# Performance work log

Measured on AMD Instinct MI355X. Metric: run time of the kernel, lower is better.

## Reference

```python
import jax, jax.numpy as jnp
import numpy as np

HEADS, K = 8, 32
EPS = 1e-5


def bn(x, gamma, beta):
    # batch-stat BN over all axes except the last (channel) axis
    axes = tuple(range(x.ndim - 1))
    m = jnp.mean(x, axes, keepdims=True)
    v = jnp.var(x, axes, keepdims=True)
    return (x - m) / jnp.sqrt(v + EPS) * gamma + beta


def leaky(z):
    return jax.nn.leaky_relu(z, 0.2)


def conv1(t, W, g, b):  # 1x1 Conv1d + BN + LeakyReLU, channels-last
    return leaky(bn(jnp.einsum('bnc,dc->bnd', t, W), g, b))


def conv2(t, W, g, b):  # 1x1 Conv2d + BN + LeakyReLU on (B,N,k,C)
    return leaky(bn(jnp.einsum('bnkc,dc->bnkd', t, W), g, b))


def _forward(x, pos, Wq, gq, bq, Wk, gk, bk, Wv, gv, bv,
             Wpb, gpb, bpb, We1, ge1, be1, We2, ge2, be2,
             Wm1, gm1, bm1, Wm2, gm2, bm2):
    B, N, C = x.shape
    cph = C // HEADS
    q = conv1(x, Wq, gq, bq)
    key = conv1(x, Wk, gk, bk)
    val = conv1(x, Wv, gv, bv)
    # kNN in key-feature space (DGCNN-style get_graph_feature, edge_function='global')
    sq = jnp.sum(key * key, -1)                          # (B,N)
    dist = sq[:, :, None] + sq[:, None, :] - 2.0 * jnp.einsum('bnc,bmc->bnm', key, key)
    _, idx = jax.lax.top_k(-dist, K)                     # (B,N,K)
    bidx = jnp.arange(B)[:, None, None]
    key_nb = key[bidx, idx]                              # (B,N,K,C)
    val_nb = val[bidx, idx]
    pos_nb = pos[bidx, idx]
    mask = jnp.sign(idx + 1).astype(x.dtype)             # (B,N,K), all ones for valid knn
    masked_pos = (pos_nb - pos[:, :, None, :]) * mask[..., None]
    posb = conv2(masked_pos, Wpb, gpb, bpb)              # (B,N,K,C)
    vector = key_nb - q[:, :, None, :] + posb            # vector attention logits input
    value = val_nb + posb
    vector = conv2(conv2(vector, We1, ge1, be1), We2, ge2, be2)  # (B,N,K,cph)
    vector = jax.nn.softmax(vector, axis=2) * mask[..., None]    # softmax over k neighbors
    value = value.reshape(B, N, K, cph, HEADS)
    attn = jnp.einsum('bnkgh,bnkg->bngh', value, vector).reshape(B, N, C)
    x = x + attn
    h = jax.nn.silu(bn(jnp.einsum('bnc,dc->bnd', x, Wm1), gm1, bm1))
    m = jax.nn.silu(bn(jnp.einsum('bnc,dc->bnd', h, Wm2), gm2, bm2))
    return x + m


def setup_inputs():
    key = jax.random.key(0)
    ks = jax.random.split(key, 16)
    B, N, C, H = 2, 2048, 256, 512
    cph = C // HEADS
    s = 0.02
    inp = {
        'x': jax.random.normal(ks[0], (B, N, C), jnp.float32),
        'pos': jax.random.normal(ks[1], (B, N, C), jnp.float32),
        'Wq': jax.random.normal(ks[2], (C, C), jnp.float32) * s,
        'gq': jnp.ones((C,), jnp.float32), 'bq': jnp.zeros((C,), jnp.float32),
        'Wk': jax.random.normal(ks[3], (C, C), jnp.float32) * s,
        'gk': jnp.ones((C,), jnp.float32), 'bk': jnp.zeros((C,), jnp.float32),
        'Wv': jax.random.normal(ks[4], (C, C), jnp.float32) * s,
        'gv': jnp.ones((C,), jnp.float32), 'bv': jnp.zeros((C,), jnp.float32),
        'Wpb': jax.random.normal(ks[5], (C, C), jnp.float32) * s,
        'gpb': jnp.ones((C,), jnp.float32), 'bpb': jnp.zeros((C,), jnp.float32),
        'We1': jax.random.normal(ks[6], (cph, C), jnp.float32) * s,
        'ge1': jnp.ones((cph,), jnp.float32), 'be1': jnp.zeros((cph,), jnp.float32),
        'We2': jax.random.normal(ks[7], (cph, cph), jnp.float32) * s,
        'ge2': jnp.ones((cph,), jnp.float32), 'be2': jnp.zeros((cph,), jnp.float32),
        'Wm1': jax.random.normal(ks[8], (H, C), jnp.float32) * s,
        'gm1': jnp.ones((H,), jnp.float32), 'bm1': jnp.zeros((H,), jnp.float32),
        'Wm2': jax.random.normal(ks[9], (C, H), jnp.float32) * s,
        'gm2': jnp.ones((C,), jnp.float32), 'bm2': jnp.zeros((C,), jnp.float32),
    }
    return inp


def reference(x, pos, Wq, gq, bq, Wk, gk, bk, Wv, gv, bv,
              Wpb, gpb, bpb, We1, ge1, be1, We2, ge2, be2,
              Wm1, gm1, bm1, Wm2, gm2, bm2):
    return _forward(x, pos, Wq, gq, bq, Wk, gk, bk, Wv, gv, bv,
                    Wpb, gpb, bpb, We1, ge1, be1, We2, ge2, be2,
                    Wm1, gm1, bm1, Wm2, gm2, bm2)
```

## Files before the change

kernel.cpp:

```cpp
#include <hip/hip_runtime.h>

#define EPS 1e-5f

typedef __attribute__((ext_vector_type(8))) short s8v;
typedef __attribute__((ext_vector_type(4))) float f4v;

__device__ __forceinline__ float leakyf(float z){ return z >= 0.f ? z : 0.2f*z; }
__device__ __forceinline__ float siluf(float y){ return y / (1.f + __expf(-y)); }
__device__ __forceinline__ unsigned f2bfu(float f){
  unsigned u = __float_as_uint(f);
  return (u + 0x7FFFu + ((u>>16)&1u)) >> 16;
}
__device__ __forceinline__ unsigned short bfr(float f){ return (unsigned short)f2bfu(f); }
__device__ __forceinline__ float bf2f16(unsigned short s){ return __uint_as_float(((unsigned)s)<<16); }

__global__ __launch_bounds__(256) void k_zero(float* __restrict__ p, int n){
  int i = blockIdx.x*256 + threadIdx.x;
  if (i < n) p[i] = 0.f;
}

template<bool TRANSA, bool STATS, bool FULL4>
__global__ __launch_bounds__(256) void k_gemm(
    const float* __restrict__ A, int lda, long aStr,
    const float* __restrict__ A3, int lda3,
    const float* __restrict__ fAbuck, float invnA, int CA,
    const float* __restrict__ gA, const float* __restrict__ bA,
    const float* __restrict__ B0, const float* __restrict__ B1,
    const float* __restrict__ B2, const float* __restrict__ B3, int ldb, long bStr,
    float* __restrict__ C, int ldc, long cStr,
    float* __restrict__ C3, int ldc3,
    int K, float* __restrict__ buck, int statC, int statChanStr)
{
  __shared__ unsigned short Ah[2048], Al[2048], Bh[2048], Bl[2048];
  __shared__ float Ssum[STATS?64:4], Ssq[STATS?64:4];
  __shared__ float mrA[TRANSA?1024:4];
  const int z = blockIdx.z;
  const bool zAlt = (A3 != nullptr) && (z == 3);
  const float* Az = zAlt ? A3 : A + (long)z*aStr;
  const int ldaz = zAlt ? lda3 : lda;
  const float* Bb = (z==0?B0 : z==1?B1 : (z==2?B2:B3)) + (long)z*bStr;
  float* Cb = zAlt ? C3 : (C + (long)z*cStr);
  const int ldcz = zAlt ? ldc3 : ldc;
  const bool doStats = STATS && !zAlt;
  const int tid = threadIdx.x;
  const int bm = blockIdx.x*64, bn = blockIdx.y*64;
  const int wv = tid>>6, lane = tid&63;
  const int lm = lane&15, quad = lane>>4;
  if (doStats && tid<64){ Ssum[tid]=0.f; Ssq[tid]=0.f; }
  if (TRANSA){
    for (int c = tid; c < CA; c += 256){
      float s=0.f, q=0.f;
      for (int b=0;b<64;b++){ s += fAbuck[(long)b*2*CA + c]; q += fAbuck[(long)b*2*CA + CA + c]; }
      float m = s*invnA;
      float v = fmaxf(q*invnA - m*m, 0.f);
      mrA[c] = m; mrA[CA + c] = rsqrtf(v + EPS);
    }
    __syncthreads();
  }

  const int r0 = tid>>3, kg = tid&7;
  const int qk = kg>>1, j0 = (kg&1)*4;
  const int s0 = ((((r0>>4)  )*4 + qk)*16 + ((r0&15)^qk))*8 + j0;
  const int s1 = ((((r0>>4)+2)*4 + qk)*16 + ((r0&15)^qk))*8 + j0;
  const float* aP0 = Az + (long)(bm+r0)*ldaz + kg*4;
  const float* aP1 = aP0 + (long)32*ldaz;
  const float* bP0 = Bb + (long)(bn+r0)*ldb + kg*4;
  const float* bP1 = bP0 + (long)32*ldb;

  f4v acc[4];
  #pragma unroll
  for (int j=0;j<4;j++) acc[j] = (f4v){0.f,0.f,0.f,0.f};

  float4 a0 = *(const float4*)(aP0);
  float4 a1 = *(const float4*)(aP1);
  float4 b0 = *(const float4*)(bP0);
  float4 b1 = *(const float4*)(bP1);

  for (int k0=0; k0<K; k0+=32){
    float4 av0 = a0, av1 = a1;
    if (TRANSA){
      float4 m4 = *(const float4*)&mrA[k0 + kg*4];
      float4 r4 = *(const float4*)&mrA[CA + k0 + kg*4];
      float4 g4 = *(const float4*)(gA + k0 + kg*4);
      float4 b4 = *(const float4*)(bA + k0 + kg*4);
      av0.x = siluf((av0.x - m4.x)*r4.x*g4.x + b4.x);
      av0.y = siluf((av0.y - m4.y)*r4.y*g4.y + b4.y);
      av0.z = siluf((av0.z - m4.z)*r4.z*g4.z + b4.z);
      av0.w = siluf((av0.w - m4.w)*r4.w*g4.w + b4.w);
      av1.x = siluf((av1.x - m4.x)*r4.x*g4.x + b4.x);
      av1.y = siluf((av1.y - m4.y)*r4.y*g4.y + b4.y);
      av1.z = siluf((av1.z - m4.z)*r4.z*g4.z + b4.z);
      av1.w = siluf((av1.w - m4.w)*r4.w*g4.w + b4.w);
    }
    ushort4 h4, l4;
    h4.x=bfr(av0.x); l4.x=bfr(av0.x-bf2f16(h4.x));
    h4.y=bfr(av0.y); l4.y=bfr(av0.y-bf2f16(h4.y));
    h4.z=bfr(av0.z); l4.z=bfr(av0.z-bf2f16(h4.z));
    h4.w=bfr(av0.w); l4.w=bfr(av0.w-bf2f16(h4.w));
    *(ushort4*)&Ah[s0]=h4; *(ushort4*)&Al[s0]=l4;
    h4.x=bfr(av1.x); l4.x=bfr(av1.x-bf2f16(h4.x));
    h4.y=bfr(av1.y); l4.y=bfr(av1.y-bf2f16(h4.y));
    h4.z=bfr(av1.z); l4.z=bfr(av1.z-bf2f16(h4.z));
    h4.w=bfr(av1.w); l4.w=bfr(av1.w-bf2f16(h4.w));
    *(ushort4*)&Ah[s1]=h4; *(ushort4*)&Al[s1]=l4;
    h4.x=bfr(b0.x); l4.x=bfr(b0.x-bf2f16(h4.x));
    h4.y=bfr(b0.y); l4.y=bfr(b0.y-bf2f16(h4.y));
    h4.z=bfr(b0.z); l4.z=bfr(b0.z-bf2f16(h4.z));
    h4.w=bfr(b0.w); l4.w=bfr(b0.w-bf2f16(h4.w));
    *(ushort4*)&Bh[s0]=h4; *(ushort4*)&Bl[s0]=l4;
    h4.x=bfr(b1.x); l4.x=bfr(b1.x-bf2f16(h4.x));
    h4.y=bfr(b1.y); l4.y=bfr(b1.y-bf2f16(h4.y));
    h4.z=bfr(b1.z); l4.z=bfr(b1.z-bf2f16(h4.z));
    h4.w=bfr(b1.w); l4.w=bfr(b1.w-bf2f16(h4.w));
    *(ushort4*)&Bh[s1]=h4; *(ushort4*)&Bl[s1]=l4;
    __syncthreads();
    if (k0+32 < K){
      a0 = *(const float4*)(aP0 + k0+32);
      a1 = *(const float4*)(aP1 + k0+32);
      b0 = *(const float4*)(bP0 + k0+32);
      b1 = *(const float4*)(bP1 + k0+32);
    }
    const int soA = ((wv*4 + quad)*16 + (lm^quad))*8;
    s8v ah = *(const s8v*)&Ah[soA];
    s8v al = *(const s8v*)&Al[soA];
    #pragma unroll
    for (int j=0;j<4;j++){
      const int soB = ((j*4 + quad)*16 + (lm^quad))*8;
      s8v bh = *(const s8v*)&Bh[soB];
      s8v bl = *(const s8v*)&Bl[soB];
      acc[j] = __builtin_amdgcn_mfma_f32_16x16x32_bf16(ah, bh, acc[j], 0,0,0);
      acc[j] = __builtin_amdgcn_mfma_f32_16x16x32_bf16(ah, bl, acc[j], 0,0,0);
      acc[j] = __builtin_amdgcn_mfma_f32_16x16x32_bf16(al, bh, acc[j], 0,0,0);
      if (FULL4)
        acc[j] = __builtin_amdgcn_mfma_f32_16x16x32_bf16(al, bl, acc[j], 0,0,0);
    }
    __syncthreads();
  }
  #pragma unroll
  for (int rr=0;rr<4;rr++){
    float* cr = Cb + (long)(bm + wv*16 + quad*4 + rr)*ldcz + bn + lm;
    #pragma unroll
    for (int j=0;j<4;j++) cr[j*16] = acc[j][rr];
  }
  if (doStats){
    #pragma unroll
    for (int j=0;j<4;j++){
      float s=0.f, q=0.f;
      #pragma unroll
      for (int rr=0;rr<4;rr++){ float v = acc[j][rr]; s += v; q += v*v; }
      s += __shfl_xor(s,16,64); s += __shfl_xor(s,32,64);
      q += __shfl_xor(q,16,64); q += __shfl_xor(q,32,64);
      if (quad==0){ atomicAdd(&Ssum[j*16+lm], s); atomicAdd(&Ssq[j*16+lm], q); }
    }
    __syncthreads();
    if (tid < 64){
      int chan = statChanStr*z + bn + tid;
      float* bb = buck + (long)(blockIdx.x & 63)*2*statC;
      atomicAdd(&bb[chan], Ssum[tid]);
      atomicAdd(&bb[statC + chan], Ssq[tid]);
    }
  }
}

__global__ void k_finalize(const float* __restrict__ buck, int C, float invn, float* __restrict__ mr){
  int c = blockIdx.x*256 + threadIdx.x;
  if (c < C){
    float s=0,q=0;
    for (int b=0;b<64;b++){ s += buck[(long)b*2*C + c]; q += buck[(long)b*2*C + C + c]; }
    float m = s*invn;
    float v = fmaxf(q*invn - m*m, 0.f);
    mr[c] = m; mr[C+c] = rsqrtf(v + EPS);
  }
}

__global__ __launch_bounds__(256) void k_apply_qkv(const float* __restrict__ raw, const float* __restrict__ bQKV,
    const float* __restrict__ gq, const float* __restrict__ bq,
    const float* __restrict__ gk, const float* __restrict__ bk,
    const float* __restrict__ gv, const float* __restrict__ bv,
    float* __restrict__ key, float* __restrict__ qv, float* __restrict__ sq){
  __shared__ float mrs[1536];
  __shared__ float red[4];
  const int tid = threadIdx.x;
  const int wv = tid>>6, lane = tid&63;
  for (int c = tid; c < 768; c += 256){
    float s=0.f, q=0.f;
    for (int b=0;b<64;b++){ s += bQKV[(long)b*1536 + c]; q += bQKV[(long)b*1536 + 768 + c]; }
    float m = s*(1.f/4096.f);
    float v = fmaxf(q*(1.f/4096.f) - m*m, 0.f);
    mrs[c] = m; mrs[768+c] = rsqrtf(v + EPS);
  }
  __syncthreads();
  const float gqv = gq[tid], bqv = bq[tid], gkv = gk[tid], bkv = bk[tid], gvv = gv[tid], bvv = bv[tid];
  for (int rr=0; rr<8; rr++){
    const long r = (long)blockIdx.x*8 + rr;
    const float* row = raw + r*768;
    float zq = row[tid], zk = row[256+tid], zv = row[512+tid];
    float yq = leakyf((zq - mrs[tid])*mrs[768+tid]*gqv + bqv);
    float yk = leakyf((zk - mrs[256+tid])*mrs[1024+tid]*gkv + bkv);
    float yv = leakyf((zv - mrs[512+tid])*mrs[1280+tid]*gvv + bvv);
    qv[r*512 + tid] = yq;
    key[r*256 + tid] = yk;
    qv[r*512 + 256 + tid] = yv;
    float kq = yk*yk;
    kq += __shfl_xor(kq,1,64); kq += __shfl_xor(kq,2,64);
    kq += __shfl_xor(kq,4,64); kq += __shfl_xor(kq,8,64);
    kq += __shfl_xor(kq,16,64); kq += __shfl_xor(kq,32,64);
    if (lane==0) red[wv] = kq;
    __syncthreads();
    if (tid==0) sq[r] = red[0]+red[1]+red[2]+red[3];
    __syncthreads();
  }
}

__global__ __launch_bounds__(256) void k_topk(const float* __restrict__ G2, const float* __restrict__ sq,
    int* __restrict__ idxb, const float* __restrict__ P, float* __restrict__ bPB){
  __shared__ float dist[4][2048];
  const int wv = threadIdx.x >> 6, lane = threadIdx.x & 63;
  const int row = blockIdx.x*4 + wv;
  const int b = row >> 11, n = row & 2047;
  const float* Grow = G2 + (long)b*4194304 + (long)n*2048;
  const float* sqb = sq + b*2048;
  const float sqn = sqb[n];
  float lmin = 3.4e38f; int lidx = 0;
  for (int j=0;j<32;j++){
    int m = lane + j*64;
    float d = sqn + sqb[m] - 2.f*Grow[m];
    dist[wv][m] = d;
    if (d < lmin){ lmin = d; lidx = m; }
  }
  int* orow = idxb + row*32;
  int myidx[32];
  for (int t=0;t<32;t++){
    float v = lmin; int i = lidx;
    for (int off=32; off; off>>=1){
      float v2 = __shfl_xor(v, off, 64);
      int i2 = __shfl_xor(i, off, 64);
      if (v2 < v || (v2 == v && i2 < i)){ v = v2; i = i2; }
    }
    myidx[t] = i;
    if (lane == 0) orow[t] = i;
    if ((i & 63) == lane){
      dist[wv][i] = 3.4e38f;
      lmin = 3.4e38f; lidx = 0;
      for (int j=0;j<32;j++){
        int m = lane + j*64;
        float d = dist[wv][m];
        if (d < lmin){ lmin = d; lidx = m; }
      }
    }
  }
  const long base = (long)b << 11;
  const int c4 = lane*4;
  float4 pn = *(const float4*)(P + (long)row*256 + c4);
  float s0=0,s1=0,s2=0,s3=0,q0=0,q1=0,q2=0,q3=0;
  for (int t=0;t<32;t++){
    float4 pg = *(const float4*)(P + (base + myidx[t])*256 + c4);
    float z0 = pg.x - pn.x, z1 = pg.y - pn.y, z2 = pg.z - pn.z, z3 = pg.w - pn.w;
    s0+=z0; q0+=z0*z0; s1+=z1; q1+=z1*z1;
    s2+=z2; q2+=z2*z2; s3+=z3; q3+=z3*z3;
  }
  float* bb = bPB + (long)(blockIdx.x & 63)*512;
  atomicAdd(&bb[c4+0], s0); atomicAdd(&bb[c4+1], s1);
  atomicAdd(&bb[c4+2], s2); atomicAdd(&bb[c4+3], s3);
  atomicAdd(&bb[256+c4+0], q0); atomicAdd(&bb[256+c4+1], q1);
  atomicAdd(&bb[256+c4+2], q2); atomicAdd(&bb[256+c4+3], q3);
}

__global__ __launch_bounds__(256) void k_e1m(
    const float* __restrict__ key, const float* __restrict__ qv, const float* __restrict__ P,
    const int* __restrict__ idx, const float* __restrict__ mrPB,
    const float* __restrict__ gpb, const float* __restrict__ bpb,
    const float* __restrict__ We1, float* __restrict__ E1, float* __restrict__ buckE1)
{
  __shared__ unsigned short Ab[16384];
  __shared__ unsigned short Wb[8192];
  __shared__ float Ssum[32], Ssq[32];
  const int tid = threadIdx.x;
  const int wv = tid>>6, lane = tid&63;
  const int quad = lane>>4, lm = lane&15;
  const int bn0 = blockIdx.x*2;
  if (tid < 32){ Ssum[tid]=0.f; Ssq[tid]=0.f; }
  for (int e = tid; e < 8192; e += 256){
    int d = e >> 8, c = e & 255;
    int off = (((d>>4)*8 + (c>>5))*4 + ((c>>3)&3))*128 + (d&15)*8 + (c&7);
    Wb[off] = bfr(We1[e]);
  }
  {
    const int bn = bn0 + (wv>>1);
    const long base = (long)(bn >> 11) << 11;
    const int c4 = lane*4;
    float4 q4  = *(const float4*)(qv + (long)bn*512 + c4);
    float4 pn4 = *(const float4*)(P + (long)bn*256 + c4);
    float4 mp4 = *(const float4*)(mrPB + c4);
    float4 rp4 = *(const float4*)(mrPB + 256 + c4);
    float4 g4  = *(const float4*)(gpb + c4);
    float4 b4  = *(const float4*)(bpb + c4);
    const int ksc = c4>>5, quadc = (c4>>3)&3, jc = c4&7;
    for (int j = 0; j < 16; ++j){
      const int rloc = wv*16 + j;
      const int kk = rloc & 31;
      const int g = idx[bn*32 + kk];
      float4 kb = *(const float4*)(key + (base+g)*256 + c4);
      float4 pb = *(const float4*)(P + (base+g)*256 + c4);
      float o0 = kb.x - q4.x + leakyf((pb.x - pn4.x - mp4.x)*rp4.x*g4.x + b4.x);
      float o1 = kb.y - q4.y + leakyf((pb.y - pn4.y - mp4.y)*rp4.y*g4.y + b4.y);
      float o2 = kb.z - q4.z + leakyf((pb.z - pn4.z - mp4.z)*rp4.z*g4.z + b4.z);
      float o3 = kb.w - q4.w + leakyf((pb.w - pn4.w - mp4.w)*rp4.w*g4.w + b4.w);
      const int atile = rloc >> 4;
      const int slot = ((rloc & 15) ^ (ksc<<1) ^ quadc) & 15;
      const int off = ((atile*8 + ksc)*4 + quadc)*128 + slot*8 + jc;
      ushort4 u; u.x = bfr(o0); u.y = bfr(o1); u.z = bfr(o2); u.w = bfr(o3);
      *(ushort4*)&Ab[off] = u;
    }
  }
  __syncthreads();
  f4v acc0 = (f4v){0,0,0,0}, acc1 = (f4v){0,0,0,0};
  #pragma unroll
  for (int ks=0; ks<8; ks++){
    const int aslot = (lm ^ (ks<<1) ^ quad) & 15;
    s8v a  = *(const s8v*)&Ab[((wv*8 + ks)*4 + quad)*128 + aslot*8];
    s8v b0 = *(const s8v*)&Wb[((ks)*4 + quad)*128 + lm*8];
    s8v b1 = *(const s8v*)&Wb[((8 + ks)*4 + quad)*128 + lm*8];
    acc0 = __builtin_amdgcn_mfma_f32_16x16x32_bf16(a, b0, acc0, 0,0,0);
    acc1 = __builtin_amdgcn_mfma_f32_16x16x32_bf16(a, b1, acc1, 0,0,0);
  }
  {
    const int bn = bn0 + (wv>>1);
    const int mt = wv & 1;
    #pragma unroll
    for (int rr=0; rr<4; rr++){
      int krow = mt*16 + quad*4 + rr;
      float* o = E1 + ((long)bn*32 + krow)*32;
      o[lm]      = acc0[rr];
      o[16 + lm] = acc1[rr];
    }
  }
  float s0=0,q0=0,s1=0,q1=0;
  #pragma unroll
  for (int rr=0; rr<4; rr++){
    s0 += acc0[rr]; q0 += acc0[rr]*acc0[rr];
    s1 += acc1[rr]; q1 += acc1[rr]*acc1[rr];
  }
  s0 += __shfl_xor(s0,16,64); s0 += __shfl_xor(s0,32,64);
  q0 += __shfl_xor(q0,16,64); q0 += __shfl_xor(q0,32,64);
  s1 += __shfl_xor(s1,16,64); s1 += __shfl_xor(s1,32,64);
  q1 += __shfl_xor(q1,16,64); q1 += __shfl_xor(q1,32,64);
  if (quad == 0){
    atomicAdd(&Ssum[lm], s0);      atomicAdd(&Ssq[lm], q0);
    atomicAdd(&Ssum[16+lm], s1);   atomicAdd(&Ssq[16+lm], q1);
  }
  __syncthreads();
  if (tid < 32){
    float* bb = buckE1 + (long)(blockIdx.x & 63)*64;
    atomicAdd(&bb[tid], Ssum[tid]); atomicAdd(&bb[32+tid], Ssq[tid]);
  }
}

__global__ __launch_bounds__(256) void k_e2m(
    float* __restrict__ E, const float* __restrict__ bE1buck,
    const float* __restrict__ ge1, const float* __restrict__ be1,
    const float* __restrict__ We2, float* __restrict__ buckE2)
{
  __shared__ unsigned short Ab[8192];
  __shared__ unsigned short Wb[1024];
  __shared__ float Ssum[32], Ssq[32];
  __shared__ float mrE1s[64];
  const int tid = threadIdx.x;
  const int wv = tid>>6, lane = tid&63;
  const int quad = lane>>4, lm = lane&15;
  const long r0 = (long)blockIdx.x*256;
  if (tid < 32){
    Ssum[tid]=0.f; Ssq[tid]=0.f;
    float s=0.f, q=0.f;
    for (int b=0;b<64;b++){ s += bE1buck[b*64+tid]; q += bE1buck[b*64+32+tid]; }
    float m = s*(1.f/131072.f);
    float v = fmaxf(q*(1.f/131072.f) - m*m, 0.f);
    mrE1s[tid] = m; mrE1s[32+tid] = rsqrtf(v + EPS);
  }
  for (int e = tid; e < 1024; e += 256){
    int d = e>>5, c = e&31;
    int off = ((d>>4)*4 + ((c>>3)&3))*128 + (d&15)*8 + (c&7);
    Wb[off] = bfr(We2[e]);
  }
  __syncthreads();
  #pragma unroll
  for (int it=0; it<8; it++){
    int e = (tid + it*256)*4;
    int row = e>>5, c = e&31;
    float4 v = *(const float4*)(E + (r0 + row)*32 + c);
    float4 m4 = *(const float4*)&mrE1s[c];
    float4 r4 = *(const float4*)&mrE1s[32+c];
    float4 g4 = *(const float4*)(ge1 + c);
    float4 b4 = *(const float4*)(be1 + c);
    float o0 = leakyf((v.x - m4.x)*r4.x*g4.x + b4.x);
    float o1 = leakyf((v.y - m4.y)*r4.y*g4.y + b4.y);
    float o2 = leakyf((v.z - m4.z)*r4.z*g4.z + b4.z);
    float o3 = leakyf((v.w - m4.w)*r4.w*g4.w + b4.w);
    int quadc = (c>>3)&3, jc = c&7;
    int slot = ((row&15) ^ quadc) & 15;
    int off = ((row>>4)*4 + quadc)*128 + slot*8 + jc;
    ushort4 u; u.x=bfr(o0); u.y=bfr(o1); u.z=bfr(o2); u.w=bfr(o3);
    *(ushort4*)&Ab[off] = u;
  }
  __syncthreads();
  f4v acc0[4], acc1[4];
  #pragma unroll
  for (int i=0;i<4;i++){ acc0[i]=(f4v){0,0,0,0}; acc1[i]=(f4v){0,0,0,0}; }
  const int aslot = (lm ^ quad) & 15;
  s8v b0 = *(const s8v*)&Wb[(quad)*128 + lm*8];
  s8v b1 = *(const s8v*)&Wb[(4 + quad)*128 + lm*8];
  #pragma unroll
  for (int i=0;i<4;i++){
    const int atile = wv*4 + i;
    s8v a = *(const s8v*)&Ab[(atile*4 + quad)*128 + aslot*8];
    acc0[i] = __builtin_amdgcn_mfma_f32_16x16x32_bf16(a, b0, acc0[i], 0,0,0);
    acc1[i] = __builtin_amdgcn_mfma_f32_16x16x32_bf16(a, b1, acc1[i], 0,0,0);
  }
  __syncthreads();
  float s0=0,q0=0,s1=0,q1=0;
  #pragma unroll
  for (int i=0;i<4;i++){
    const int atile = wv*4 + i;
    #pragma unroll
    for (int rr=0; rr<4; rr++){
      long row = r0 + atile*16 + quad*4 + rr;
      float* o = E + row*32;
      o[lm]      = acc0[i][rr];
      o[16 + lm] = acc1[i][rr];
      s0 += acc0[i][rr]; q0 += acc0[i][rr]*acc0[i][rr];
      s1 += acc1[i][rr]; q1 += acc1[i][rr]*acc1[i][rr];
    }
  }
  s0 += __shfl_xor(s0,16,64); s0 += __shfl_xor(s0,32,64);
  q0 += __shfl_xor(q0,16,64); q0 += __shfl_xor(q0,32,64);
  s1 += __shfl_xor(s1,16,64); s1 += __shfl_xor(s1,32,64);
  q1 += __shfl_xor(q1,16,64); q1 += __shfl_xor(q1,32,64);
  if (quad == 0){
    atomicAdd(&Ssum[lm], s0);    atomicAdd(&Ssq[lm], q0);
    atomicAdd(&Ssum[16+lm], s1); atomicAdd(&Ssq[16+lm], q1);
  }
  __syncthreads();
  if (tid < 32){
    float* bb = buckE2 + (long)(blockIdx.x & 63)*64;
    atomicAdd(&bb[tid], Ssum[tid]); atomicAdd(&bb[32+tid], Ssq[tid]);
  }
}

__global__ __launch_bounds__(256) void k_attn(
    const float* __restrict__ E2, const float* __restrict__ bE2buck,
    const float* __restrict__ ge2, const float* __restrict__ be2,
    const float* __restrict__ qv, const float* __restrict__ P, const int* __restrict__ idx,
    const float* __restrict__ mrPB, const float* __restrict__ gpb, const float* __restrict__ bpb,
    const float* __restrict__ xin, float* __restrict__ x2)
{
  __shared__ float L[4][32][33];
  __shared__ float mrE2s[64];
  const int tid = threadIdx.x;
  const int wv = tid>>6, lane = tid&63;
  if (tid < 32){
    float s=0.f, q=0.f;
    for (int b=0;b<64;b++){ s += bE2buck[b*64+tid]; q += bE2buck[b*64+32+tid]; }
    float m = s*(1.f/131072.f);
    float v = fmaxf(q*(1.f/131072.f) - m*m, 0.f);
    mrE2s[tid] = m; mrE2s[32+tid] = rsqrtf(v + EPS);
  }
  __syncthreads();
  const int bn = blockIdx.x*4 + wv;
  const long base = (long)(bn >> 11) << 11;
  for (int qq=0; qq<4; qq++){
    int e = lane*16 + qq*4;
    int k = e >> 5, g0 = e & 31;
    float4 v  = *(const float4*)(E2 + (long)bn*1024 + e);
    float4 m4 = *(const float4*)&mrE2s[g0];
    float4 r4 = *(const float4*)&mrE2s[32+g0];
    float4 g4 = *(const float4*)(ge2 + g0);
    float4 b4 = *(const float4*)(be2 + g0);
    L[wv][k][g0+0] = leakyf((v.x - m4.x)*r4.x*g4.x + b4.x);
    L[wv][k][g0+1] = leakyf((v.y - m4.y)*r4.y*g4.y + b4.y);
    L[wv][k][g0+2] = leakyf((v.z - m4.z)*r4.z*g4.z + b4.z);
    L[wv][k][g0+3] = leakyf((v.w - m4.w)*r4.w*g4.w + b4.w);
  }
  __syncthreads();
  {
    const int g = lane & 31, h = lane >> 5;
    float mx = -3.4e38f;
    for (int j=0;j<16;j++) mx = fmaxf(mx, L[wv][h*16+j][g]);
    mx = fmaxf(mx, __shfl_xor(mx, 32, 64));
    float sm = 0.f, ev[16];
    for (int j=0;j<16;j++){ float e_ = __expf(L[wv][h*16+j][g] - mx); ev[j] = e_; sm += e_; }
    sm += __shfl_xor(sm, 32, 64);
    float inv = 1.f/sm;
    for (int j=0;j<16;j++) L[wv][h*16+j][g] = ev[j]*inv;
  }
  __syncthreads();
  const int c4 = lane*4, gg = lane >> 1;
  float4 pn4 = *(const float4*)(P + (long)bn*256 + c4);
  float4 mp4 = *(const float4*)(mrPB + c4);
  float4 rp4 = *(const float4*)(mrPB + 256 + c4);
  float4 g4 = *(const float4*)(gpb + c4);
  float4 b4 = *(const float4*)(bpb + c4);
  float accv[4] = {0,0,0,0};
  const int* ir = idx + bn*32;
  for (int k=0;k<32;k++){
    int gi = ir[k];
    float4 vv = *(const float4*)(qv + (long)(base+gi)*512 + 256 + c4);
    float4 pp = *(const float4*)(P + (base+gi)*256 + c4);
    float w = L[wv][k][gg];
    float zh0 = (pp.x - pn4.x - mp4.x)*rp4.x*g4.x + b4.x;
    float zh1 = (pp.y - pn4.y - mp4.y)*rp4.y*g4.y + b4.y;
    float zh2 = (pp.z - pn4.z - mp4.z)*rp4.z*g4.z + b4.z;
    float zh3 = (pp.w - pn4.w - mp4.w)*rp4.w*g4.w + b4.w;
    accv[0] = fmaf(vv.x + leakyf(zh0), w, accv[0]);
    accv[1] = fmaf(vv.y + leakyf(zh1), w, accv[1]);
    accv[2] = fmaf(vv.z + leakyf(zh2), w, accv[2]);
    accv[3] = fmaf(vv.w + leakyf(zh3), w, accv[3]);
  }
  float4 x4 = *(const float4*)(xin + (long)bn*256 + c4);
  float4 o;
  o.x = x4.x + accv[0]; o.y = x4.y + accv[1];
  o.z = x4.z + accv[2]; o.w = x4.w + accv[3];
  *(float4*)(x2 + (long)bn*256 + c4) = o;
}

__global__ __launch_bounds__(256) void k_final(const float* __restrict__ x2, const float* __restrict__ Zm2,
    const float* __restrict__ bM2buck, const float* __restrict__ gm, const float* __restrict__ bm,
    float* __restrict__ out){
  __shared__ float mrs[512];
  const int tid = threadIdx.x;
  {
    float s=0.f, q=0.f;
    for (int b=0;b<64;b++){ s += bM2buck[(long)b*512 + tid]; q += bM2buck[(long)b*512 + 256 + tid]; }
    float m = s*(1.f/4096.f);
    float v = fmaxf(q*(1.f/4096.f) - m*m, 0.f);
    mrs[tid] = m; mrs[256+tid] = rsqrtf(v + EPS);
  }
  __syncthreads();
  const float gmv = gm[tid], bmv = bm[tid];
  #pragma unroll
  for (int rr=0; rr<8; rr++){
    long r = (long)blockIdx.x*8 + rr;
    float z = Zm2[r*256 + tid];
    float y = (z - mrs[tid])*mrs[256+tid]*gmv + bmv;
    out[r*256 + tid] = x2[r*256 + tid] + siluf(y);
  }
}

extern "C" void kernel_launch(void* const* d_in, const int* in_sizes, int n_in,
                              void* d_out, int out_size, void* d_ws, size_t ws_size,
                              hipStream_t stream){
  (void)in_sizes; (void)n_in; (void)out_size; (void)ws_size;
  const float* x   = (const float*)d_in[0];
  const float* pos = (const float*)d_in[1];
  const float* Wq  = (const float*)d_in[2];
  const float* gq  = (const float*)d_in[3];
  const float* bq  = (const float*)d_in[4];
  const float* Wk  = (const float*)d_in[5];
  const float* gk  = (const float*)d_in[6];
  const float* bk  = (const float*)d_in[7];
  const float* Wv  = (const float*)d_in[8];
  const float* gv  = (const float*)d_in[9];
  const float* bv  = (const float*)d_in[10];
  const float* Wpb = (const float*)d_in[11];
  const float* gpb = (const float*)d_in[12];
  const float* bpb = (const float*)d_in[13];
  const float* We1 = (const float*)d_in[14];
  const float* ge1 = (const float*)d_in[15];
  const float* be1 = (const float*)d_in[16];
  const float* We2 = (const float*)d_in[17];
  const float* ge2 = (const float*)d_in[18];
  const float* be2 = (const float*)d_in[19];
  const float* Wm1 = (const float*)d_in[20];
  const float* gm1 = (const float*)d_in[21];
  const float* bm1 = (const float*)d_in[22];
  const float* Wm2 = (const float*)d_in[23];
  const float* gm2 = (const float*)d_in[24];
  const float* bm2 = (const float*)d_in[25];

  float* w     = (float*)d_ws;
  float* arena = w;
  float* key   = w + 4194304;
  float* P     = w + 5242880;
  float* x2    = w + 6291456;
  float* qv    = w + 7340032;
  float* sq    = w + 9437184;
  int*   idx   = (int*)(w + 9441280);
  float* buck  = w + 9572352;
  float* mr    = w + 9809920;
  float* G2    = w + 9813632;
  float* bQKV = buck;            float* bPB = buck + 98304;  float* bE1 = buck + 131072;
  float* bE2  = buck + 135168;   float* bM1 = buck + 139264; float* bM2 = buck + 204800;
  float* mrPB = mr + 1536;
  float* Zm1 = arena;
  float* Zm2 = arena + 2097152;

  k_zero<<<928,256,0,stream>>>(buck, 237568);
  k_gemm<false,true,true><<<dim3(64,4,4),256,0,stream>>>(
      x,256,0, pos,256, nullptr,0.f,0, nullptr,nullptr,
      Wq,Wk,Wv,Wpb,256,0, arena,768,256, P,256, 256, bQKV,768,256);
  k_apply_qkv<<<512,256,0,stream>>>(arena, bQKV, gq,bq,gk,bk,gv,bv, key, qv, sq);
  k_gemm<false,false,true><<<dim3(32,32,2),256,0,stream>>>(
      key,256,524288, nullptr,0, nullptr,0.f,0, nullptr,nullptr,
      key,key,key,nullptr,256,524288, G2,2048,4194304, nullptr,0, 256, nullptr,0,0);
  k_topk<<<1024,256,0,stream>>>(G2, sq, idx, P, bPB);
  k_finalize<<<1,256,0,stream>>>(bPB, 256, 1.f/131072.f, mrPB);
  k_e1m<<<2048,256,0,stream>>>(key, qv, P, idx, mrPB, gpb, bpb, We1, arena, bE1);
  k_e2m<<<512,256,0,stream>>>(arena, bE1, ge1, be1, We2, bE2);
  k_attn<<<1024,256,0,stream>>>(arena, bE2, ge2, be2, qv, P, idx, mrPB, gpb, bpb, x, x2);
  k_gemm<false,true,false><<<dim3(64,8,1),256,0,stream>>>(
      x2,256,0, nullptr,0, nullptr,0.f,0, nullptr,nullptr,
      Wm1,Wm1,Wm1,nullptr,256,0, Zm1,512,0, nullptr,0, 256, bM1,512,0);
  k_gemm<true,true,false><<<dim3(64,4,1),256,0,stream>>>(
      Zm1,512,0, nullptr,0, bM1,1.f/4096.f,512, gm1,bm1,
      Wm2,Wm2,Wm2,nullptr,512,0, Zm2,256,0, nullptr,0, 512, bM2,256,0);
  k_final<<<512,256,0,stream>>>(x2, Zm2, bM2, gm2, bm2, (float*)d_out);
}
```

Measured before the change: 358.1 us.

## Replace iterative argmin top-k with per-lane bitonic sort and wave merge

Each lane packs its 32 candidate distances with their indices into 64-bit sortable keys and bitonic-sorts them in registers. The sorted lists go to shared memory, and the wave extracts the top 32 by repeatedly taking a shuffle-reduced minimum over the lanes' list heads. The winning lane then advances its pointer instead of rescanning 32 shared-memory entries after every pick. This trades the serial rescan for a large unrolled sorting network and higher register use from the 32 64-bit keys, which may lower occupancy.

```diff
diff --git a/kernel.cpp b/kernel.cpp
--- a/kernel.cpp
+++ b/kernel.cpp
@@ -214,47 +214,78 @@
 
 __global__ __launch_bounds__(256) void k_topk(const float* __restrict__ G2, const float* __restrict__ sq,
     int* __restrict__ idxb, const float* __restrict__ P, float* __restrict__ bPB){
-  __shared__ float dist[4][2048];
+  __shared__ float Vs[4*2112];
+  __shared__ unsigned short Is[4*2112];
   const int wv = threadIdx.x >> 6, lane = threadIdx.x & 63;
   const int row = blockIdx.x*4 + wv;
   const int b = row >> 11, n = row & 2047;
   const float* Grow = G2 + (long)b*4194304 + (long)n*2048;
   const float* sqb = sq + b*2048;
   const float sqn = sqb[n];
-  float lmin = 3.4e38f; int lidx = 0;
+  unsigned long long key[32];
+  #pragma unroll
   for (int j=0;j<32;j++){
     int m = lane + j*64;
     float d = sqn + sqb[m] - 2.f*Grow[m];
-    dist[wv][m] = d;
-    if (d < lmin){ lmin = d; lidx = m; }
-  }
+    unsigned u = __float_as_uint(d);
+    u ^= ((unsigned)((int)u >> 31)) | 0x80000000u;
+    key[j] = ((unsigned long long)u << 32) | (unsigned)m;
+  }
+  #pragma unroll
+  for (int k=2;k<=32;k<<=1){
+    #pragma unroll
+    for (int jj=k>>1;jj>0;jj>>=1){
+      #pragma unroll
+      for (int ii=0;ii<32;ii++){
+        int ll = ii ^ jj;
+        if (ll > ii){
+          bool up = ((ii & k) == 0);
+          unsigned long long a = key[ii], c = key[ll];
+          bool sw = (a > c) == up;
+          key[ii] = sw ? c : a;
+          key[ll] = sw ? a : c;
+        }
+      }
+    }
+  }
+  const int base = wv*2112 + lane*33;
+  #pragma unroll
+  for (int t=0;t<32;t++){
+    Vs[base+t] = __uint_as_float((unsigned)(key[t] >> 32));
+    Is[base+t] = (unsigned short)(key[t] & 0xFFFFu);
+  }
+  unsigned long long hkey = key[0];
+  int ptr = 1;
   int* orow = idxb + row*32;
   int myidx[32];
+  #pragma unroll
   for (int t=0;t<32;t++){
-    float v = lmin; int i = lidx;
+    unsigned long long v = hkey;
+    #pragma unroll
     for (int off=32; off; off>>=1){
-      float v2 = __shfl_xor(v, off, 64);
-      int i2 = __shfl_xor(i, off, 64);
-      if (v2 < v || (v2 == v && i2 < i)){ v = v2; i = i2; }
-    }
-    myidx[t] = i;
-    if (lane == 0) orow[t] = i;
-    if ((i & 63) == lane){
-      dist[wv][i] = 3.4e38f;
-      lmin = 3.4e38f; lidx = 0;
-      for (int j=0;j<32;j++){
-        int m = lane + j*64;
-        float d = dist[wv][m];
-        if (d < lmin){ lmin = d; lidx = m; }
+      unsigned long long v2 = (unsigned long long)__shfl_xor((long long)v, off, 64);
+      if (v2 < v) v = v2;
+    }
+    int wi = (int)(v & 0xFFFFFFFFull);
+    myidx[t] = wi;
+    if (lane == 0) orow[t] = wi;
+    if (v == hkey){
+      if (ptr < 32){
+        unsigned uu = __float_as_uint(Vs[base+ptr]);
+        hkey = ((unsigned long long)uu << 32) | Is[base+ptr];
+      } else {
+        hkey = 0xFFFFFFFFFFFFFFFFull;
       }
-    }
-  }
-  const long base = (long)b << 11;
+      ptr++;
+    }
+  }
+  const long bbase = (long)b << 11;
   const int c4 = lane*4;
   float4 pn = *(const float4*)(P + (long)row*256 + c4);
   float s0=0,s1=0,s2=0,s3=0,q0=0,q1=0,q2=0,q3=0;
+  #pragma unroll
   for (int t=0;t<32;t++){
-    float4 pg = *(const float4*)(P + (base + myidx[t])*256 + c4);
+    float4 pg = *(const float4*)(P + (bbase + myidx[t])*256 + c4);
     float z0 = pg.x - pn.x, z1 = pg.y - pn.y, z2 = pg.z - pn.z, z3 = pg.w - pn.w;
     s0+=z0; q0+=z0*z0; s1+=z1; q1+=z1*z1;
     s2+=z2; q2+=z2*z2; s3+=z3; q3+=z3*z3;
```

New measurement: 346.7 us. -3.2%, faster.

## Keep per-lane top-4 packed keys in kNN selection to avoid rescans

Applied to the files above, without the earlier changes.

Rewrites the per-row top-k selection so each lane keeps a sorted list of its 4 smallest distances, packed as 64-bit keys (order-preserving distance bits plus index). The wave reduction then needs one 64-bit shuffle-min per step instead of separate value and index shuffles with a tiebreak. The winning lane pops from its list and only rescans its 32 entries in shared memory once the list is empty. Winner indices go to shared memory instead of a per-thread 32-entry array, which avoids register or scratch spilling.

```diff
diff --git a/kernel.cpp b/kernel.cpp
--- a/kernel.cpp
+++ b/kernel.cpp
@@ -214,47 +214,68 @@
 
 __global__ __launch_bounds__(256) void k_topk(const float* __restrict__ G2, const float* __restrict__ sq,
     int* __restrict__ idxb, const float* __restrict__ P, float* __restrict__ bPB){
-  __shared__ float dist[4][2048];
+  __shared__ unsigned Ds[4][2048];
+  __shared__ int Ws[4][32];
   const int wv = threadIdx.x >> 6, lane = threadIdx.x & 63;
   const int row = blockIdx.x*4 + wv;
   const int b = row >> 11, n = row & 2047;
   const float* Grow = G2 + (long)b*4194304 + (long)n*2048;
   const float* sqb = sq + b*2048;
   const float sqn = sqb[n];
-  float lmin = 3.4e38f; int lidx = 0;
+  const unsigned long long SEN = 0xFFFFFFFFFFFFFFFFull;
+  unsigned long long k0=SEN,k1=SEN,k2=SEN,k3=SEN;
+  #pragma unroll
   for (int j=0;j<32;j++){
     int m = lane + j*64;
     float d = sqn + sqb[m] - 2.f*Grow[m];
-    dist[wv][m] = d;
-    if (d < lmin){ lmin = d; lidx = m; }
+    unsigned u = __float_as_uint(d);
+    u ^= ((unsigned)((int)u >> 31)) | 0x80000000u;
+    Ds[wv][m] = u;
+    unsigned long long kk = ((unsigned long long)u << 32) | (unsigned)m;
+    if (kk < k3){
+      k3 = kk;
+      if (k3 < k2){ unsigned long long t_=k2; k2=k3; k3=t_; }
+      if (k2 < k1){ unsigned long long t_=k1; k1=k2; k2=t_; }
+      if (k1 < k0){ unsigned long long t_=k0; k0=k1; k1=t_; }
+    }
   }
   int* orow = idxb + row*32;
-  int myidx[32];
   for (int t=0;t<32;t++){
-    float v = lmin; int i = lidx;
+    unsigned long long v = k0;
+    #pragma unroll
     for (int off=32; off; off>>=1){
-      float v2 = __shfl_xor(v, off, 64);
-      int i2 = __shfl_xor(i, off, 64);
-      if (v2 < v || (v2 == v && i2 < i)){ v = v2; i = i2; }
-    }
-    myidx[t] = i;
-    if (lane == 0) orow[t] = i;
-    if ((i & 63) == lane){
-      dist[wv][i] = 3.4e38f;
-      lmin = 3.4e38f; lidx = 0;
-      for (int j=0;j<32;j++){
-        int m = lane + j*64;
-        float d = dist[wv][m];
-        if (d < lmin){ lmin = d; lidx = m; }
+      unsigned long long v2 = (unsigned long long)__shfl_xor((long long)v, off, 64);
+      if (v2 < v) v = v2;
+    }
+    int wi = (int)(v & 0xFFFFFFFFull);
+    if (lane == 0){ orow[t] = wi; Ws[wv][t] = wi; }
+    if (v == k0){
+      Ds[wv][wi] = 0xFFFFFFFFu;
+      k0=k1; k1=k2; k2=k3; k3=SEN;
+      if (k0 == SEN){
+        for (int j=0;j<32;j++){
+          int m = lane + j*64;
+          unsigned u = Ds[wv][m];
+          if (u != 0xFFFFFFFFu){
+            unsigned long long kk = ((unsigned long long)u << 32) | (unsigned)m;
+            if (kk < k3){
+              k3 = kk;
+              if (k3 < k2){ unsigned long long t_=k2; k2=k3; k3=t_; }
+              if (k2 < k1){ unsigned long long t_=k1; k1=k2; k2=t_; }
+              if (k1 < k0){ unsigned long long t_=k0; k0=k1; k1=t_; }
+            }
+          }
+        }
       }
     }
   }
-  const long base = (long)b << 11;
+  const long bbase = (long)b << 11;
   const int c4 = lane*4;
   float4 pn = *(const float4*)(P + (long)row*256 + c4);
   float s0=0,s1=0,s2=0,s3=0,q0=0,q1=0,q2=0,q3=0;
+  #pragma unroll
   for (int t=0;t<32;t++){
-    float4 pg = *(const float4*)(P + (base + myidx[t])*256 + c4);
+    float4 pg = *(const float4*)(P + (bbase + Ws[wv][t])*256 + c4);
     float z0 = pg.x - pn.x, z1 = pg.y - pn.y, z2 = pg.z - pn.z, z3 = pg.w - pn.w;
     s0+=z0; q0+=z0*z0; s1+=z1; q1+=z1*z1;
     s2+=z2; q2+=z2*z2; s3+=z3; q3+=z3*z3;
```

Measured after the change: 344.2 us. -3.9%, faster.
